# Kernel optimization log

Hardware: AMD Instinct MI355X
Metric: run time of the kernel (lower is better)

Reference implementation:

```python
import jax, jax.numpy as jnp
import numpy as np

N, E = 50000, 800000
D_IN_N, D_IN_E, D_OUT = 64, 64, 64


def setup_inputs() -> dict:
    key = jax.random.key(0)
    ks = jax.random.split(key, 10)
    stdv = 1.0 / np.sqrt(D_OUT)
    u = lambda k, shape: jax.random.uniform(k, shape, jnp.float32, -stdv, stdv)
    return {
        "nf": jax.random.normal(ks[0], (N, D_IN_N), jnp.float32),
        "ef": jax.random.normal(ks[1], (E, D_IN_E), jnp.float32),
        "src": jax.random.randint(ks[2], (E,), 0, N, jnp.int32),
        "dst": jax.random.randint(ks[3], (E,), 0, N, jnp.int32),
        "W_node": u(ks[4], (D_IN_N, D_OUT)),
        "W_edge": u(ks[5], (D_IN_E, D_OUT)),
        "bias_node": u(ks[6], (D_OUT,)),
        "bias_edge": u(ks[7], (D_OUT,)),
        "W_dense": u(ks[8], (2 * D_OUT, D_OUT)),  # Linear(2*out, out) weight, stored transposed
        "b_dense": u(ks[9], (D_OUT,)),
    }


def reference(nf, ef, src, dst, W_node, W_edge, bias_node, bias_edge, W_dense, b_dense):
    n_nodes = nf.shape[0]
    # input projections
    nf_h = nf @ W_node                     # [N, D]
    ef_h = ef @ W_edge                     # [E, D]
    # update_all: mean of incoming edge features per dst node (0 for isolated nodes, DGL default)
    deg = jax.ops.segment_sum(jnp.ones((ef_h.shape[0],), ef_h.dtype), dst, num_segments=n_nodes)
    nb_ef = jax.ops.segment_sum(ef_h, dst, num_segments=n_nodes) / jnp.maximum(deg, 1.0)[:, None]
    # apply_nodes: nf = act(nf + bias)
    nf_out = jax.nn.relu(nf_h + bias_node)
    # apply_edges (uses updated nf): cat([ef + nb_ef[dst], (nf[src]+nf[dst])/2]) -> Linear -> +bias -> act
    tmp_ef = ef_h + nb_ef[dst]             # [E, D]
    srcdst_nf = (nf_out[src] + nf_out[dst]) * 0.5
    ef_out = jnp.concatenate([tmp_ef, srcdst_nf], axis=1) @ W_dense + b_dense + bias_edge
    ef_out = jax.nn.relu(ef_out)
    return nf_out, ef_out
```

## Files before the change

kernel.cpp:

```cpp
#include <hip/hip_runtime.h>

#define D 64

typedef __attribute__((ext_vector_type(8))) short short8;
typedef __attribute__((ext_vector_type(4))) float f32x4;

__device__ __forceinline__ ushort f2b(float f) {
    union { float f; unsigned u; } x; x.f = f;
    unsigned r = x.u + 0x7FFFu + ((x.u >> 16) & 1u);
    return (ushort)(r >> 16);
}
__device__ __forceinline__ float b2f(ushort u) {
    union { float f; unsigned u; } x; x.u = ((unsigned)u) << 16;
    return x.f;
}
__device__ __forceinline__ short8 pack8(float4 a, float4 b) {
    short8 r;
    r[0] = (short)f2b(a.x); r[1] = (short)f2b(a.y); r[2] = (short)f2b(a.z); r[3] = (short)f2b(a.w);
    r[4] = (short)f2b(b.x); r[5] = (short)f2b(b.y); r[6] = (short)f2b(b.z); r[7] = (short)f2b(b.w);
    return r;
}

#define LDA 72

__global__ __launch_bounds__(256) void fused_front_kernel(
    const float* __restrict__ nf, const float* __restrict__ Wn,
    const float* __restrict__ bias, const float* __restrict__ Wd,
    float* __restrict__ out, ushort* __restrict__ nfp_b, int N,
    const int* __restrict__ dst, int* __restrict__ deg_i, int E,
    const float* __restrict__ W_edge, const float* __restrict__ b_dense,
    const float* __restrict__ bias_edge, ushort* __restrict__ Wcomb_b,
    float* __restrict__ bias2, int NPB, int HB)
{
    __shared__ ushort Bn[64 * LDA];
    __shared__ ushort Bd[64 * LDA];
    __shared__ ushort Vs[64 * LDA];
    const int tid = threadIdx.x;
    const int bid = blockIdx.x;

    if (bid < NPB) {
        const long row0 = (long)bid * 64;
        const int w = tid >> 6, lane = tid & 63;
        const int lr = lane & 15, g = lane >> 4;
        const bool odd = lane & 1;

        {
            int k = tid >> 2, n0 = (tid & 3) * 16;
            const float4* wr = (const float4*)(Wn + (long)k * D + n0);
            float4 v0 = wr[0], v1 = wr[1], v2 = wr[2], v3 = wr[3];
            float vs[16] = {v0.x, v0.y, v0.z, v0.w, v1.x, v1.y, v1.z, v1.w,
                            v2.x, v2.y, v2.z, v2.w, v3.x, v3.y, v3.z, v3.w};
            #pragma unroll
            for (int j = 0; j < 16; ++j) Bn[(n0 + j) * LDA + k] = f2b(vs[j]);
            const float4* wd = (const float4*)(Wd + (long)(D + k) * D + n0);
            float4 u0 = wd[0], u1 = wd[1], u2 = wd[2], u3 = wd[3];
            float us[16] = {u0.x, u0.y, u0.z, u0.w, u1.x, u1.y, u1.z, u1.w,
                            u2.x, u2.y, u2.z, u2.w, u3.x, u3.y, u3.z, u3.w};
            #pragma unroll
            for (int j = 0; j < 16; ++j) Bd[(n0 + j) * LDA + k] = f2b(0.5f * us[j]);
        }

        long era = row0 + 16 * w + lr; if (era >= N) era = N - 1;
        const float4* ap = (const float4*)(nf + era * D);
        float4 v0 = ap[2 * g], v1 = ap[2 * g + 1];
        float4 v2 = ap[8 + 2 * g], v3 = ap[8 + 2 * g + 1];
        short8 a0 = pack8(v0, v1), a1 = pack8(v2, v3);
        __syncthreads();

        f32x4 acc[4];
        #pragma unroll
        for (int t = 0; t < 4; ++t) {
            f32x4 z = {0.f, 0.f, 0.f, 0.f};
            short8 b0 = *(const short8*)&Bn[(16 * t + lr) * LDA + 8 * g];
            short8 b1 = *(const short8*)&Bn[(16 * t + lr) * LDA + 32 + 8 * g];
            z = __builtin_amdgcn_mfma_f32_16x16x32_bf16(a0, b0, z, 0, 0, 0);
            z = __builtin_amdgcn_mfma_f32_16x16x32_bf16(a1, b1, z, 0, 0, 0);
            acc[t] = z;
        }
        #pragma unroll
        for (int t = 0; t < 4; ++t) {
            int c = 16 * t + lr;
            float bb = bias[c];
            #pragma unroll
            for (int reg = 0; reg < 4; ++reg) {
                int r = 16 * w + 4 * g + reg;
                float v = fmaxf(acc[t][reg] + bb, 0.f);
                long rg = row0 + r;
                if (rg < N) out[rg * D + c] = v;
                Vs[r * LDA + c] = f2b(v);
            }
        }
        __syncthreads();

        short8 c0 = *(const short8*)&Vs[(16 * w + lr) * LDA + 8 * g];
        short8 c1 = *(const short8*)&Vs[(16 * w + lr) * LDA + 32 + 8 * g];
        f32x4 acc2[4];
        #pragma unroll
        for (int t = 0; t < 4; ++t) {
            f32x4 z = {0.f, 0.f, 0.f, 0.f};
            short8 b0 = *(const short8*)&Bd[(16 * t + lr) * LDA + 8 * g];
            short8 b1 = *(const short8*)&Bd[(16 * t + lr) * LDA + 32 + 8 * g];
            z = __builtin_amdgcn_mfma_f32_16x16x32_bf16(c0, b0, z, 0, 0, 0);
            z = __builtin_amdgcn_mfma_f32_16x16x32_bf16(c1, b1, z, 0, 0, 0);
            acc2[t] = z;
        }
        const int rb = 16 * w + 4 * g + (odd ? 2 : 0);
        long e0 = row0 + rb, e1 = row0 + rb + 1;
        #pragma unroll
        for (int t = 0; t < 4; ++t) {
            float p0 = __shfl_xor(acc2[t][0], 1, 64);
            float p1 = __shfl_xor(acc2[t][1], 1, 64);
            float p2 = __shfl_xor(acc2[t][2], 1, 64);
            float p3 = __shfl_xor(acc2[t][3], 1, 64);
            float lo0, hi0, lo1, hi1;
            if (odd) { lo0 = p2; hi0 = acc2[t][2]; lo1 = p3; hi1 = acc2[t][3]; }
            else     { lo0 = acc2[t][0]; hi0 = p0; lo1 = acc2[t][1]; hi1 = p1; }
            int cbase = 16 * t + (lr & ~1);
            unsigned dw0 = ((unsigned)f2b(hi0) << 16) | (unsigned)f2b(lo0);
            unsigned dw1 = ((unsigned)f2b(hi1) << 16) | (unsigned)f2b(lo1);
            if (e0 < N) *(unsigned*)(nfp_b + e0 * D + cbase) = dw0;
            if (e1 < N) *(unsigned*)(nfp_b + e1 * D + cbase) = dw1;
        }
    } else if (bid < NPB + HB) {
        int i = (bid - NPB) * 256 + tid;
        if (i < E) atomicAdd(deg_i + dst[i], 1);
    } else {
        for (int idx = tid; idx < D * D; idx += 256) {
            int k = idx >> 6, n = idx & 63;
            float s = 0.f;
            #pragma unroll 8
            for (int j = 0; j < D; ++j)
                s = fmaf(W_edge[k * D + j], Wd[j * D + n], s);
            Wcomb_b[n * D + k] = f2b(s);
        }
        if (tid < D) bias2[tid] = b_dense[tid] + bias_edge[tid];
    }
}

__global__ __launch_bounds__(256) void scanA_kernel(
    const int* __restrict__ deg_i, int* __restrict__ pos,
    int* __restrict__ bsum, int N)
{
    __shared__ int s[256];
    const int tid = threadIdx.x;
    const int i = blockIdx.x * 256 + tid;
    int v = (i < N) ? deg_i[i] : 0;
    s[tid] = v;
    __syncthreads();
    #pragma unroll
    for (int off = 1; off < 256; off <<= 1) {
        int t = (tid >= off) ? s[tid - off] : 0;
        __syncthreads();
        s[tid] += t;
        __syncthreads();
    }
    if (i < N) pos[i] = s[tid] - v;
    if (tid == 255) bsum[blockIdx.x] = s[255];
}

__global__ __launch_bounds__(256) void scanB_kernel(int* __restrict__ bsum, int NB)
{
    __shared__ int s[256];
    const int tid = threadIdx.x;
    int v = (tid < NB) ? bsum[tid] : 0;
    s[tid] = v;
    __syncthreads();
    #pragma unroll
    for (int off = 1; off < 256; off <<= 1) {
        int t = (tid >= off) ? s[tid - off] : 0;
        __syncthreads();
        s[tid] += t;
        __syncthreads();
    }
    if (tid < NB) bsum[tid] = s[tid] - v;
}

__global__ __launch_bounds__(256) void scatter_kernel(
    const int* __restrict__ dst, const int* __restrict__ src,
    const int* __restrict__ pos, const int* __restrict__ bsum,
    int* __restrict__ cnt, int4* __restrict__ sorted_eds, int E)
{
    int i = blockIdx.x * 256 + threadIdx.x;
    if (i < E) {
        int dv = dst[i];
        int slot = pos[dv] + bsum[dv >> 8] + atomicAdd(cnt + dv, 1);
        sorted_eds[slot] = make_int4(i, dv, src[i], 0);
    }
}

#define SEG_ROWS 256
#define SLSTR 34
__global__ __launch_bounds__(256) void efp_seg_kernel(
    const float* __restrict__ ef, const int4* __restrict__ sorted_eds,
    const ushort* __restrict__ Wt, ushort* __restrict__ efp,
    float* __restrict__ nb_sum, int E)
{
    __shared__ unsigned Slds[SEG_ROWS * SLSTR];
    __shared__ int dsts[SEG_ROWS];
    const int tid = threadIdx.x;
    const long s0 = (long)blockIdx.x * SEG_ROWS;

    const int w = tid >> 6, lane = tid & 63;
    const int lr = lane & 15, g = lane >> 4;
    const bool odd = lane & 1;

    long gde[4];
    #pragma unroll
    for (int tt = 0; tt < 4; ++tt) {
        long s = s0 + 64 * tt + 16 * w + lr;
        if (s >= E) s = E - 1;
        gde[tt] = (long)sorted_eds[s].x;
    }
    float4 va[4][4];
    #pragma unroll
    for (int tt = 0; tt < 4; ++tt) {
        const float4* ap = (const float4*)(ef + gde[tt] * D);
        va[tt][0] = ap[2 * g];     va[tt][1] = ap[2 * g + 1];
        va[tt][2] = ap[8 + 2 * g]; va[tt][3] = ap[8 + 2 * g + 1];
    }
    {
        long s = s0 + tid;
        dsts[tid] = (s < E) ? sorted_eds[s].y : -1;
    }

    short8 bf0[4], bf1[4];
    #pragma unroll
    for (int t = 0; t < 4; ++t) {
        bf0[t] = *(const short8*)&Wt[(16 * t + lr) * D + 8 * g];
        bf1[t] = *(const short8*)&Wt[(16 * t + lr) * D + 32 + 8 * g];
    }

    #pragma unroll
    for (int tt = 0; tt < 4; ++tt) {
        short8 a0 = pack8(va[tt][0], va[tt][1]);
        short8 a1 = pack8(va[tt][2], va[tt][3]);
        f32x4 acc[4];
        #pragma unroll
        for (int t = 0; t < 4; ++t) {
            f32x4 z = {0.f, 0.f, 0.f, 0.f};
            z = __builtin_amdgcn_mfma_f32_16x16x32_bf16(a0, bf0[t], z, 0, 0, 0);
            z = __builtin_amdgcn_mfma_f32_16x16x32_bf16(a1, bf1[t], z, 0, 0, 0);
            acc[t] = z;
        }

        const int rb = 64 * tt + 16 * w + 4 * g + (odd ? 2 : 0);
        long sl0 = s0 + rb, sl1 = s0 + rb + 1;
        #pragma unroll
        for (int t = 0; t < 4; ++t) {
            float p0 = __shfl_xor(acc[t][0], 1, 64);
            float p1 = __shfl_xor(acc[t][1], 1, 64);
            float p2 = __shfl_xor(acc[t][2], 1, 64);
            float p3 = __shfl_xor(acc[t][3], 1, 64);
            float lo0, hi0, lo1, hi1;
            if (odd) { lo0 = p2; hi0 = acc[t][2]; lo1 = p3; hi1 = acc[t][3]; }
            else     { lo0 = acc[t][0]; hi0 = p0; lo1 = acc[t][1]; hi1 = p1; }
            int cbase = 16 * t + (lr & ~1);
            int dc = cbase >> 1;
            unsigned dw0 = ((unsigned)f2b(hi0) << 16) | (unsigned)f2b(lo0);
            unsigned dw1 = ((unsigned)f2b(hi1) << 16) | (unsigned)f2b(lo1);
            if (sl0 < E) *(unsigned*)(efp + sl0 * D + cbase) = dw0;
            if (sl1 < E) *(unsigned*)(efp + sl1 * D + cbase) = dw1;
            Slds[rb * SLSTR + dc]       = dw0;
            Slds[(rb + 1) * SLSTR + dc] = dw1;
        }
    }
    __syncthreads();

    {
        const int dwc = tid & 31;
        const int r0 = (tid >> 5) * 32;
        float seg0 = 0.f, seg1 = 0.f;
        int cur = dsts[r0];
        #pragma unroll 4
        for (int r = r0; r < r0 + 32; ++r) {
            int dv = dsts[r];
            unsigned u = Slds[r * SLSTR + dwc];
            if (dv != cur) {
                if (cur >= 0) {
                    atomicAdd(nb_sum + (long)cur * D + 2 * dwc, seg0);
                    atomicAdd(nb_sum + (long)cur * D + 2 * dwc + 1, seg1);
                }
                seg0 = seg1 = 0.f;
                cur = dv;
            }
            seg0 += b2f((ushort)(u & 0xffff));
            seg1 += b2f((ushort)(u >> 16));
        }
        if (cur >= 0) {
            atomicAdd(nb_sum + (long)cur * D + 2 * dwc, seg0);
            atomicAdd(nb_sum + (long)cur * D + 2 * dwc + 1, seg1);
        }
    }
}

__global__ __launch_bounds__(256) void final_kernel(
    const ushort* __restrict__ efp, const int4* __restrict__ sorted_eds,
    const float* __restrict__ nb_sum, const int* __restrict__ deg_i,
    const ushort* __restrict__ nfp_b, const float* __restrict__ bias2,
    float* __restrict__ out, int E)
{
    long idx = (long)blockIdx.x * 256 + threadIdx.x;
    long s = idx >> 2;
    int q = (int)(idx & 3);
    if (s >= E) return;
    int4 ed = sorted_eds[s];
    long eid = ed.x;
    int dv = ed.y, sv = ed.z;

    const short8* ep = (const short8*)(efp + s * D + q * 16);
    const float4* nb = (const float4*)(nb_sum + (long)dv * D + q * 16);
    const short8* nd = (const short8*)(nfp_b + (long)dv * D + q * 16);
    const short8* sp = (const short8*)(nfp_b + (long)sv * D + q * 16);
    short8 e0 = ep[0], e1 = ep[1];
    float4 x0 = nb[0], x1 = nb[1], x2 = nb[2], x3 = nb[3];
    short8 d0 = nd[0], d1 = nd[1];
    short8 s0 = sp[0], s1 = sp[1];
    float inv = 1.0f / fmaxf((float)deg_i[dv], 1.0f);
    const float4* bp = (const float4*)(bias2 + q * 16);
    float4 b0 = bp[0], b1 = bp[1], b2 = bp[2], b3 = bp[3];

    float xb[16] = {x0.x, x0.y, x0.z, x0.w, x1.x, x1.y, x1.z, x1.w,
                    x2.x, x2.y, x2.z, x2.w, x3.x, x3.y, x3.z, x3.w};
    float r[16];
    #pragma unroll
    for (int j = 0; j < 8; ++j) {
        r[j]     = b2f((ushort)e0[j]) + xb[j] * inv + b2f((ushort)d0[j]) + b2f((ushort)s0[j]);
        r[8 + j] = b2f((ushort)e1[j]) + xb[8 + j] * inv + b2f((ushort)d1[j]) + b2f((ushort)s1[j]);
    }
    float4* op = (float4*)(out + eid * D + q * 16);
    op[0] = make_float4(fmaxf(r[0] + b0.x, 0.f), fmaxf(r[1] + b0.y, 0.f),
                        fmaxf(r[2] + b0.z, 0.f), fmaxf(r[3] + b0.w, 0.f));
    op[1] = make_float4(fmaxf(r[4] + b1.x, 0.f), fmaxf(r[5] + b1.y, 0.f),
                        fmaxf(r[6] + b1.z, 0.f), fmaxf(r[7] + b1.w, 0.f));
    op[2] = make_float4(fmaxf(r[8] + b2.x, 0.f), fmaxf(r[9] + b2.y, 0.f),
                        fmaxf(r[10] + b2.z, 0.f), fmaxf(r[11] + b2.w, 0.f));
    op[3] = make_float4(fmaxf(r[12] + b3.x, 0.f), fmaxf(r[13] + b3.y, 0.f),
                        fmaxf(r[14] + b3.z, 0.f), fmaxf(r[15] + b3.w, 0.f));
}

extern "C" void kernel_launch(void* const* d_in, const int* in_sizes, int n_in,
                              void* d_out, int out_size, void* d_ws, size_t ws_size,
                              hipStream_t stream) {
    const float* nf        = (const float*)d_in[0];
    const float* ef        = (const float*)d_in[1];
    const int*   src       = (const int*)d_in[2];
    const int*   dst       = (const int*)d_in[3];
    const float* W_node    = (const float*)d_in[4];
    const float* W_edge    = (const float*)d_in[5];
    const float* bias_node = (const float*)d_in[6];
    const float* bias_edge = (const float*)d_in[7];
    const float* W_dense   = (const float*)d_in[8];
    const float* b_dense   = (const float*)d_in[9];

    const int N = in_sizes[0] / D;
    const int E = in_sizes[1] / D;
    const int NB = (N + 255) / 256;
    const int NPB = (N + 63) / 64;
    const int HB = (E + 255) / 256;

    float* nf_out = (float*)d_out;
    float* ef_out = (float*)d_out + (size_t)N * D;

    char* p = (char*)d_ws;
    int*    deg_i    = (int*)p;     p += (size_t)N * 4;
    float*  nb_sum   = (float*)p;   p += (size_t)N * D * 4;
    int*    cnt      = (int*)p;     p += (size_t)N * 4;
    size_t  zbytes   = (size_t)(p - (char*)d_ws);
    int*    pos      = (int*)p;     p += (size_t)N * 4;
    int*    bsum     = (int*)p;     p += 256 * 4;
    int4*   sorted_eds=(int4*)p;    p += (size_t)E * 16;
    ushort* nfp_b    = (ushort*)p;  p += (size_t)N * D * 2;
    ushort* Wcomb_b  = (ushort*)p;  p += D * D * 2;
    float*  bias2    = (float*)p;   p += 256;
    ushort* efp      = (ushort*)p;

    hipMemsetAsync(d_ws, 0, zbytes, stream);

    fused_front_kernel<<<NPB + HB + 1, 256, 0, stream>>>(
        nf, W_node, bias_node, W_dense, nf_out, nfp_b, N,
        dst, deg_i, E, W_edge, b_dense, bias_edge, Wcomb_b, bias2, NPB, HB);
    scanA_kernel<<<NB, 256, 0, stream>>>(deg_i, pos, bsum, N);
    scanB_kernel<<<1, 256, 0, stream>>>(bsum, NB);
    scatter_kernel<<<(E + 255) / 256, 256, 0, stream>>>(dst, src, pos, bsum, cnt,
                                                        sorted_eds, E);
    efp_seg_kernel<<<(E + SEG_ROWS - 1) / SEG_ROWS, 256, 0, stream>>>(
        ef, sorted_eds, Wcomb_b, efp, nb_sum, E);
    final_kernel<<<(int)(((size_t)E * 4 + 255) / 256), 256, 0, stream>>>(
        efp, sorted_eds, nb_sum, deg_i, nfp_b, bias2, ef_out, E);
}
```

Baseline: 331.2 us.

## Replace atomic segment sums with per-node CSR mean kernel producing bf16 node term

Removes the LDS segmented reduction and float atomicAdds into nb_sum from the MFMA kernel. A new per-node kernel walks each node's contiguous sorted edge range, computes the mean, adds the node projection, and stores a bf16 per-node term. The final kernel then reads one bf16 row per dst instead of an fp32 nb_sum row plus a bf16 node row and the degree. The packed int4 sorted edge records are also split into an eid array and an int2 (dst, src) array. The cost is an extra launch and a second read of efp, plus bf16 rounding of the combined node term.

Measured after the change: 339.7 us. +2.6%, slower.

```diff
diff --git a/kernel.cpp b/kernel.cpp
--- a/kernel.cpp
+++ b/kernel.cpp
@@ -178,28 +178,25 @@
 __global__ __launch_bounds__(256) void scatter_kernel(
     const int* __restrict__ dst, const int* __restrict__ src,
     const int* __restrict__ pos, const int* __restrict__ bsum,
-    int* __restrict__ cnt, int4* __restrict__ sorted_eds, int E)
+    int* __restrict__ cnt, int* __restrict__ sorted_eid,
+    int2* __restrict__ sorted_ds, int E)
 {
     int i = blockIdx.x * 256 + threadIdx.x;
     if (i < E) {
         int dv = dst[i];
         int slot = pos[dv] + bsum[dv >> 8] + atomicAdd(cnt + dv, 1);
-        sorted_eds[slot] = make_int4(i, dv, src[i], 0);
+        sorted_eid[slot] = i;
+        sorted_ds[slot] = make_int2(dv, src[i]);
     }
 }
 
 #define SEG_ROWS 256
-#define SLSTR 34
-__global__ __launch_bounds__(256) void efp_seg_kernel(
-    const float* __restrict__ ef, const int4* __restrict__ sorted_eds,
-    const ushort* __restrict__ Wt, ushort* __restrict__ efp,
-    float* __restrict__ nb_sum, int E)
-{
-    __shared__ unsigned Slds[SEG_ROWS * SLSTR];
-    __shared__ int dsts[SEG_ROWS];
+__global__ __launch_bounds__(256) void efp_mfma_kernel(
+    const float* __restrict__ ef, const int* __restrict__ sorted_eid,
+    const ushort* __restrict__ Wt, ushort* __restrict__ efp, int E)
+{
     const int tid = threadIdx.x;
     const long s0 = (long)blockIdx.x * SEG_ROWS;
-
     const int w = tid >> 6, lane = tid & 63;
     const int lr = lane & 15, g = lane >> 4;
     const bool odd = lane & 1;
@@ -209,7 +206,7 @@
     for (int tt = 0; tt < 4; ++tt) {
         long s = s0 + 64 * tt + 16 * w + lr;
         if (s >= E) s = E - 1;
-        gde[tt] = (long)sorted_eds[s].x;
+        gde[tt] = (long)sorted_eid[s];
     }
     float4 va[4][4];
     #pragma unroll
@@ -217,10 +214,6 @@
         const float4* ap = (const float4*)(ef + gde[tt] * D);
         va[tt][0] = ap[2 * g];     va[tt][1] = ap[2 * g + 1];
         va[tt][2] = ap[8 + 2 * g]; va[tt][3] = ap[8 + 2 * g + 1];
-    }
-    {
-        long s = s0 + tid;
-        dsts[tid] = (s < E) ? sorted_eds[s].y : -1;
     }
 
     short8 bf0[4], bf1[4];
@@ -255,47 +248,48 @@
             if (odd) { lo0 = p2; hi0 = acc[t][2]; lo1 = p3; hi1 = acc[t][3]; }
             else     { lo0 = acc[t][0]; hi0 = p0; lo1 = acc[t][1]; hi1 = p1; }
             int cbase = 16 * t + (lr & ~1);
-            int dc = cbase >> 1;
             unsigned dw0 = ((unsigned)f2b(hi0) << 16) | (unsigned)f2b(lo0);
             unsigned dw1 = ((unsigned)f2b(hi1) << 16) | (unsigned)f2b(lo1);
             if (sl0 < E) *(unsigned*)(efp + sl0 * D + cbase) = dw0;
             if (sl1 < E) *(unsigned*)(efp + sl1 * D + cbase) = dw1;
-            Slds[rb * SLSTR + dc]       = dw0;
-            Slds[(rb + 1) * SLSTR + dc] = dw1;
-        }
-    }
-    __syncthreads();
-
-    {
-        const int dwc = tid & 31;
-        const int r0 = (tid >> 5) * 32;
-        float seg0 = 0.f, seg1 = 0.f;
-        int cur = dsts[r0];
-        #pragma unroll 4
-        for (int r = r0; r < r0 + 32; ++r) {
-            int dv = dsts[r];
-            unsigned u = Slds[r * SLSTR + dwc];
-            if (dv != cur) {
-                if (cur >= 0) {
-                    atomicAdd(nb_sum + (long)cur * D + 2 * dwc, seg0);
-                    atomicAdd(nb_sum + (long)cur * D + 2 * dwc + 1, seg1);
-                }
-                seg0 = seg1 = 0.f;
-                cur = dv;
-            }
-            seg0 += b2f((ushort)(u & 0xffff));
-            seg1 += b2f((ushort)(u >> 16));
-        }
-        if (cur >= 0) {
-            atomicAdd(nb_sum + (long)cur * D + 2 * dwc, seg0);
-            atomicAdd(nb_sum + (long)cur * D + 2 * dwc + 1, seg1);
-        }
+        }
+    }
+}
+
+__global__ __launch_bounds__(256) void segmean_ndp_kernel(
+    const ushort* __restrict__ efp, const int* __restrict__ pos,
+    const int* __restrict__ bsum, const int* __restrict__ deg_i,
+    const ushort* __restrict__ nfp_b, ushort* __restrict__ ndp_b, int N)
+{
+    const int w = threadIdx.x >> 6, lane = threadIdx.x & 63;
+    const int n = blockIdx.x * 4 + w;
+    if (n >= N) return;
+    const int rp = lane >> 5, dc = lane & 31;
+    const long p0 = (long)pos[n] + bsum[n >> 8];
+    const int d = deg_i[n];
+
+    float seg0 = 0.f, seg1 = 0.f;
+    for (int i = rp; i < d; i += 2) {
+        unsigned u = *(const unsigned*)(efp + (p0 + i) * D + dc * 2);
+        seg0 += b2f((ushort)(u & 0xffff));
+        seg1 += b2f((ushort)(u >> 16));
+    }
+    seg0 += __shfl_xor(seg0, 32, 64);
+    seg1 += __shfl_xor(seg1, 32, 64);
+
+    if (rp == 0) {
+        float inv = 1.0f / fmaxf((float)d, 1.0f);
+        unsigned nu = *(const unsigned*)(nfp_b + (long)n * D + dc * 2);
+        float r0 = seg0 * inv + b2f((ushort)(nu & 0xffff));
+        float r1 = seg1 * inv + b2f((ushort)(nu >> 16));
+        unsigned dw = ((unsigned)f2b(r1) << 16) | (unsigned)f2b(r0);
+        *(unsigned*)(ndp_b + (long)n * D + dc * 2) = dw;
     }
 }
 
 __global__ __launch_bounds__(256) void final_kernel(
-    const ushort* __restrict__ efp, const int4* __restrict__ sorted_eds,
-    const float* __restrict__ nb_sum, const int* __restrict__ deg_i,
+    const ushort* __restrict__ efp, const int* __restrict__ sorted_eid,
+    const int2* __restrict__ sorted_ds, const ushort* __restrict__ ndp_b,
     const ushort* __restrict__ nfp_b, const float* __restrict__ bias2,
     float* __restrict__ out, int E)
 {
@@ -303,29 +297,24 @@
     long s = idx >> 2;
     int q = (int)(idx & 3);
     if (s >= E) return;
-    int4 ed = sorted_eds[s];
-    long eid = ed.x;
-    int dv = ed.y, sv = ed.z;
+    long eid = sorted_eid[s];
+    int2 ds = sorted_ds[s];
+    int dv = ds.x, sv = ds.y;
 
     const short8* ep = (const short8*)(efp + s * D + q * 16);
-    const float4* nb = (const float4*)(nb_sum + (long)dv * D + q * 16);
-    const short8* nd = (const short8*)(nfp_b + (long)dv * D + q * 16);
+    const short8* np = (const short8*)(ndp_b + (long)dv * D + q * 16);
     const short8* sp = (const short8*)(nfp_b + (long)sv * D + q * 16);
     short8 e0 = ep[0], e1 = ep[1];
-    float4 x0 = nb[0], x1 = nb[1], x2 = nb[2], x3 = nb[3];
-    short8 d0 = nd[0], d1 = nd[1];
+    short8 n0 = np[0], n1 = np[1];
     short8 s0 = sp[0], s1 = sp[1];
-    float inv = 1.0f / fmaxf((float)deg_i[dv], 1.0f);
     const float4* bp = (const float4*)(bias2 + q * 16);
     float4 b0 = bp[0], b1 = bp[1], b2 = bp[2], b3 = bp[3];
 
-    float xb[16] = {x0.x, x0.y, x0.z, x0.w, x1.x, x1.y, x1.z, x1.w,
-                    x2.x, x2.y, x2.z, x2.w, x3.x, x3.y, x3.z, x3.w};
     float r[16];
     #pragma unroll
     for (int j = 0; j < 8; ++j) {
-        r[j]     = b2f((ushort)e0[j]) + xb[j] * inv + b2f((ushort)d0[j]) + b2f((ushort)s0[j]);
-        r[8 + j] = b2f((ushort)e1[j]) + xb[8 + j] * inv + b2f((ushort)d1[j]) + b2f((ushort)s1[j]);
+        r[j]     = b2f((ushort)e0[j]) + b2f((ushort)n0[j]) + b2f((ushort)s0[j]);
+        r[8 + j] = b2f((ushort)e1[j]) + b2f((ushort)n1[j]) + b2f((ushort)s1[j]);
     }
     float4* op = (float4*)(out + eid * D + q * 16);
     op[0] = make_float4(fmaxf(r[0] + b0.x, 0.f), fmaxf(r[1] + b0.y, 0.f),
@@ -363,13 +352,14 @@
 
     char* p = (char*)d_ws;
     int*    deg_i    = (int*)p;     p += (size_t)N * 4;
-    float*  nb_sum   = (float*)p;   p += (size_t)N * D * 4;
     int*    cnt      = (int*)p;     p += (size_t)N * 4;
     size_t  zbytes   = (size_t)(p - (char*)d_ws);
     int*    pos      = (int*)p;     p += (size_t)N * 4;
     int*    bsum     = (int*)p;     p += 256 * 4;
-    int4*   sorted_eds=(int4*)p;    p += (size_t)E * 16;
+    int*    sorted_eid=(int*)p;     p += (size_t)E * 4;
+    int2*   sorted_ds= (int2*)p;    p += (size_t)E * 8;
     ushort* nfp_b    = (ushort*)p;  p += (size_t)N * D * 2;
+    ushort* ndp_b    = (ushort*)p;  p += (size_t)N * D * 2;
     ushort* Wcomb_b  = (ushort*)p;  p += D * D * 2;
     float*  bias2    = (float*)p;   p += 256;
     ushort* efp      = (ushort*)p;
@@ -382,9 +372,11 @@
     scanA_kernel<<<NB, 256, 0, stream>>>(deg_i, pos, bsum, N);
     scanB_kernel<<<1, 256, 0, stream>>>(bsum, NB);
     scatter_kernel<<<(E + 255) / 256, 256, 0, stream>>>(dst, src, pos, bsum, cnt,
-                                                        sorted_eds, E);
-    efp_seg_kernel<<<(E + SEG_ROWS - 1) / SEG_ROWS, 256, 0, stream>>>(
-        ef, sorted_eds, Wcomb_b, efp, nb_sum, E);
+                                                        sorted_eid, sorted_ds, E);
+    efp_mfma_kernel<<<(E + SEG_ROWS - 1) / SEG_ROWS, 256, 0, stream>>>(
+        ef, sorted_eid, Wcomb_b, efp, E);
+    segmean_ndp_kernel<<<(N + 3) / 4, 256, 0, stream>>>(
+        efp, pos, bsum, deg_i, nfp_b, ndp_b, N);
     final_kernel<<<(int)(((size_t)E * 4 + 255) / 256), 256, 0, stream>>>(
-        efp, sorted_eds, nb_sum, deg_i, nfp_b, bias2, ef_out, E);
-}
+        efp, sorted_eid, sorted_ds, ndp_b, nfp_b, bias2, ef_out, E);
+}
```
